# Performance work log

Measured on AMD Instinct MI355X. Metric: run time of the kernel, lower is better.

## Reference

```python
import jax, jax.numpy as jnp
import numpy as np

C = 128  # n_atom_basis


def setup_inputs() -> dict:
    key = jax.random.key(0)
    k_h, k_A, k_Ww, k_Wb, k_aw, k_ab = jax.random.split(key, 6)
    B, N = 8, 2048
    h = jax.random.normal(k_h, (B, N, C), dtype=jnp.float32)
    A = jax.random.uniform(k_A, (B, N, N), dtype=jnp.float32)
    # nn.Linear(C, C)
    lim_W = 1.0 / np.sqrt(C)
    W_w = jax.random.uniform(k_Ww, (C, C), minval=-lim_W, maxval=lim_W, dtype=jnp.float32)
    W_b = jax.random.uniform(k_Wb, (C,), minval=-lim_W, maxval=lim_W, dtype=jnp.float32)
    # nn.Linear(2C, 1)
    lim_a = 1.0 / np.sqrt(2 * C)
    a_w = jax.random.uniform(k_aw, (2 * C,), minval=-lim_a, maxval=lim_a, dtype=jnp.float32)
    a_b = jax.random.uniform(k_ab, (), minval=-lim_a, maxval=lim_a, dtype=jnp.float32)
    return {"h": h, "A": A, "W_w": W_w, "W_b": W_b, "a_w": a_w, "a_b": a_b}


def reference(h, A, W_w, W_b, a_w, a_b):
    # Wh computed once ([B,N,C]) instead of the original's redundant [B,N,N,C] broadcast.
    Wh = jnp.einsum('bnc,dc->bnd', h, W_w) + W_b
    # a([hi, hj]) = a_w[:C]@Wh_i + a_w[C:]@Wh_j + a_b  -> rank-1 decomposition of the concat-linear
    si = Wh @ a_w[:C]          # [B,N]
    sj = Wh @ a_w[C:]          # [B,N]
    s = si[:, :, None] + sj[:, None, :] + a_b  # [B,N,N] raw scores
    e = jnp.exp(s) * A                          # masked exp (no max-subtraction: matches original math)
    alpha = e / jnp.sum(e, axis=2, keepdims=True)
    # weighted sum over neighbors j of the ORIGINAL h (as in the source, not Wh)
    h_prime = jnp.einsum('bij,bjc->bic', alpha, h)
    return h_prime
```

## Files before the change

kernel.cpp:

```cpp
#include <hip/hip_runtime.h>
#include <math.h>
#include <stdint.h>

#define Bn 8
#define Nn 2048
#define Cn 128
#define CP 144
#define NKB (Nn / 32)

typedef _Float16 f16x8 __attribute__((ext_vector_type(8)));
typedef _Float16 f16x4 __attribute__((ext_vector_type(4)));
typedef _Float16 f16x2 __attribute__((ext_vector_type(2)));
typedef __fp16   fp16x2 __attribute__((ext_vector_type(2)));
typedef float    f32x4 __attribute__((ext_vector_type(4)));

__global__ __launch_bounds__(256) void prep_kernel(const float* __restrict__ Ww,
                                                   const float* __restrict__ Wb,
                                                   const float* __restrict__ aw,
                                                   float* __restrict__ vout) {
    int tid = threadIdx.x;
    if (tid < 128) {
        float acc = 0.f;
#pragma unroll 16
        for (int d = 0; d < Cn; ++d) acc += Ww[d * Cn + tid] * aw[Cn + d];
        vout[tid] = acc;
    } else if (tid < 192) {
        int i = tid - 128;
        float p = Wb[i] * aw[Cn + i] + Wb[i + 64] * aw[Cn + i + 64];
        p += __shfl_xor(p, 32, 64);
        p += __shfl_xor(p, 16, 64);
        p += __shfl_xor(p, 8, 64);
        p += __shfl_xor(p, 4, 64);
        p += __shfl_xor(p, 2, 64);
        p += __shfl_xor(p, 1, 64);
        if (i == 0) vout[128] = p;
    }
}

__global__ __launch_bounds__(256) void rows_kernel(const float* __restrict__ h,
                                                   const float* __restrict__ vout,
                                                   _Float16* __restrict__ hWt) {
    __shared__ float tile[16][132];
    __shared__ float vsh[129];
    __shared__ float wsh[16];

    int bid = blockIdx.x;
    int b   = bid & 7;
    int n0  = (bid >> 3) << 4;
    int tid = threadIdx.x;

    if (tid < 129) vsh[tid] = vout[tid];
    {
#pragma unroll
        for (int i = 0; i < 2; ++i) {
            int idx = tid + 256 * i;
            int r = idx >> 5, f4 = idx & 31;
            *(float4*)&tile[r][f4 * 4] =
                ((const float4*)(h + (size_t)(b * Nn + n0 + r) * Cn))[f4];
        }
    }
    __syncthreads();

    {
        int r = tid >> 4, g = tid & 15;
        float acc = 0.f;
#pragma unroll
        for (int ii = 0; ii < 8; ++ii) {
            int i = g * 8 + ii;
            acc += tile[r][i] * vsh[i];
        }
        acc += __shfl_xor(acc, 1, 64);
        acc += __shfl_xor(acc, 2, 64);
        acc += __shfl_xor(acc, 4, 64);
        acc += __shfl_xor(acc, 8, 64);
        if (g == 0) wsh[r] = expf(acc + vsh[128]);
    }
    __syncthreads();

    {
        int kb = n0 >> 5, khalf = (n0 >> 4) & 1;
        _Float16* hWb = hWt + ((size_t)(b * NKB + kb) * CP) * 32 + khalf * 16;
#pragma unroll
        for (int i = 0; i < 5; ++i) {
            int idx = tid + 256 * i;
            if (idx < 1152) {
                int cp = idx >> 3, p = idx & 7;
                int r0 = p * 2;
                f16x2 v2;
                if (cp < 128) {
                    v2[0] = (_Float16)(wsh[r0] * tile[r0][cp]);
                    v2[1] = (_Float16)(wsh[r0 + 1] * tile[r0 + 1][cp]);
                } else if (cp == 128) {
                    v2[0] = (_Float16)wsh[r0];
                    v2[1] = (_Float16)wsh[r0 + 1];
                } else {
                    v2[0] = (_Float16)0.f;
                    v2[1] = (_Float16)0.f;
                }
                *(f16x2*)(hWb + (size_t)cp * 32 + p * 2) = v2;
            }
        }
    }
}

__global__ __launch_bounds__(512, 4) void attn_kernel(const float* __restrict__ A,
                                                      const _Float16* __restrict__ hWt,
                                                      float* __restrict__ out) {
    __shared__ _Float16 Af[2][4][32][40];
    __shared__ float den[32];

    int bid = blockIdx.x;
    int b   = bid & 7;
    int i0  = (bid >> 3) << 5;
    int tid = threadIdx.x;
    int wv  = tid >> 6, l = tid & 63;
    int m   = l & 15, q = l >> 4;

    const float*    Ab  = A   + (size_t)(b * Nn + i0) * Nn;
    const _Float16* hWb = hWt + (size_t)b * NKB * CP * 32;

    int sr0 = tid >> 5, sf4 = tid & 31;
    const float* sgA = Ab + (size_t)sr0 * Nn + sf4 * 4;
    const float* sgB = Ab + (size_t)(sr0 + 16) * Nn + sf4 * 4;
    int sch = sf4 >> 3, skl = (sf4 & 7) * 4;

    f32x4 accc[2];
    f32x4 acc8;
    accc[0] = (f32x4){0.f, 0.f, 0.f, 0.f};
    accc[1] = (f32x4){0.f, 0.f, 0.f, 0.f};
    acc8    = (f32x4){0.f, 0.f, 0.f, 0.f};

    auto cvtst = [&](int t, int row, float4 v) {
        union { fp16x2 h2[2]; f16x4 v4; } u;
        u.h2[0] = __builtin_amdgcn_cvt_pkrtz(v.x, v.y);
        u.h2[1] = __builtin_amdgcn_cvt_pkrtz(v.z, v.w);
        *(f16x4*)&Af[t & 1][sch][row][skl] = u.v4;
    };
    auto loadB = [&](int t, f16x8* bf) {
#pragma unroll
        for (int ck = 0; ck < 4; ++ck)
            bf[ck] = *(const f16x8*)(hWb + ((size_t)(4 * t + ck) * CP + wv * 16 + m) * 32 + q * 8);
        if (wv < 2) {
#pragma unroll
            for (int ck = 0; ck < 4; ++ck)
                bf[4 + ck] = *(const f16x8*)(hWb + ((size_t)(4 * t + ck) * CP + 128 + m) * 32 + q * 8);
        }
    };
    auto compute = [&](int buf, const f16x8* bf) {
#pragma unroll
        for (int ck = 0; ck < 4; ++ck) {
            f16x8 af0 = *(const f16x8*)&Af[buf][ck][m][q * 8];
            f16x8 af1 = *(const f16x8*)&Af[buf][ck][16 + m][q * 8];
            accc[0] = __builtin_amdgcn_mfma_f32_16x16x32_f16(af0, bf[ck], accc[0], 0, 0, 0);
            accc[1] = __builtin_amdgcn_mfma_f32_16x16x32_f16(af1, bf[ck], accc[1], 0, 0, 0);
            if (wv < 2)
                acc8 = __builtin_amdgcn_mfma_f32_16x16x32_f16(wv ? af1 : af0, bf[4 + ck],
                                                              acc8, 0, 0, 0);
        }
    };

    float4 a0x = *(const float4*)(sgA);
    float4 a0y = *(const float4*)(sgB);
    float4 a1x = *(const float4*)(sgA + 128);
    float4 a1y = *(const float4*)(sgB + 128);
    f16x8 bfA[8], bfB[8];
    loadB(0, bfA);
    cvtst(0, sr0, a0x);
    cvtst(0, sr0 + 16, a0y);
    __syncthreads();

    for (int t2 = 0; t2 < 8; ++t2) {
        int te = 2 * t2, to = te + 1;
        loadB(to, bfB);
        if (t2 < 7) {
            a0x = *(const float4*)(sgA + (te + 2) * 128);
            a0y = *(const float4*)(sgB + (te + 2) * 128);
        }
        compute(0, bfA);
        cvtst(to, sr0, a1x);
        cvtst(to, sr0 + 16, a1y);
        __syncthreads();
        if (t2 < 7) {
            loadB(to + 1, bfA);
            a1x = *(const float4*)(sgA + (to + 2) * 128);
            a1y = *(const float4*)(sgB + (to + 2) * 128);
        }
        compute(1, bfB);
        if (t2 < 7) {
            cvtst(to + 1, sr0, a0x);
            cvtst(to + 1, sr0 + 16, a0y);
        }
        __syncthreads();
    }

    if (wv < 2 && m == 0) {
#pragma unroll
        for (int r = 0; r < 4; ++r) den[wv * 16 + q * 4 + r] = acc8[r];
    }
    __syncthreads();

#pragma unroll
    for (int mt = 0; mt < 2; ++mt) {
#pragma unroll
        for (int r = 0; r < 4; ++r) {
            int row = mt * 16 + q * 4 + r;
            float invd = 1.f / den[row];
            out[(size_t)(b * Nn + i0 + row) * Cn + wv * 16 + m] = accc[mt][r] * invd;
        }
    }
}

extern "C" void kernel_launch(void* const* d_in, const int* in_sizes, int n_in,
                              void* d_out, int out_size, void* d_ws, size_t ws_size,
                              hipStream_t stream) {
    const float* h  = (const float*)d_in[0];
    const float* A  = (const float*)d_in[1];
    const float* Ww = (const float*)d_in[2];
    const float* Wb = (const float*)d_in[3];
    const float* aw = (const float*)d_in[4];
    float* out = (float*)d_out;

    char* ws = (char*)d_ws;
    _Float16* hWt  = (_Float16*)ws;
    float*    vout = (float*)(ws + (size_t)Bn * NKB * CP * 32 * 2);

    prep_kernel<<<1, 256, 0, stream>>>(Ww, Wb, aw, vout);
    rows_kernel<<<Bn * (Nn / 16), 256, 0, stream>>>(h, vout, hWt);
    attn_kernel<<<Bn * (Nn / 32), 512, 0, stream>>>(A, hWt, out);
}
```

Baseline: 234.8 us.

## Feed A directly into 32x32 MFMA operands, dropping LDS staging

The attention kernel now loads each wave's A fragment straight from global memory into registers, converts it to fp16 and feeds 32x32x16 MFMAs. This removes the LDS double buffer and the per-step block barriers. Each block now covers 64 rows instead of 32, and the hW buffer's padded channel dimension grows to 160 so every 32-wide channel tile lines up. The cost is that each A row is fetched by four waves (one per channel tile), relying on cache hits, and per-lane loads are strided across rows, so coalescing is worse.

New measurement: 291.0 us. 1.24x slower.

```diff
diff --git a/kernel.cpp b/kernel.cpp
--- a/kernel.cpp
+++ b/kernel.cpp
@@ -5,14 +5,14 @@
 #define Bn 8
 #define Nn 2048
 #define Cn 128
-#define CP 144
+#define CP2 160
 #define NKB (Nn / 32)
 
 typedef _Float16 f16x8 __attribute__((ext_vector_type(8)));
 typedef _Float16 f16x4 __attribute__((ext_vector_type(4)));
 typedef _Float16 f16x2 __attribute__((ext_vector_type(2)));
 typedef __fp16   fp16x2 __attribute__((ext_vector_type(2)));
-typedef float    f32x4 __attribute__((ext_vector_type(4)));
+typedef float    f32x16 __attribute__((ext_vector_type(16)));
 
 __global__ __launch_bounds__(256) void prep_kernel(const float* __restrict__ Ww,
                                                    const float* __restrict__ Wb,
@@ -79,134 +79,84 @@
 
     {
         int kb = n0 >> 5, khalf = (n0 >> 4) & 1;
-        _Float16* hWb = hWt + ((size_t)(b * NKB + kb) * CP) * 32 + khalf * 16;
+        _Float16* hWb = hWt + ((size_t)(b * NKB + kb) * CP2) * 32 + khalf * 16;
 #pragma unroll
         for (int i = 0; i < 5; ++i) {
             int idx = tid + 256 * i;
-            if (idx < 1152) {
-                int cp = idx >> 3, p = idx & 7;
-                int r0 = p * 2;
-                f16x2 v2;
-                if (cp < 128) {
-                    v2[0] = (_Float16)(wsh[r0] * tile[r0][cp]);
-                    v2[1] = (_Float16)(wsh[r0 + 1] * tile[r0 + 1][cp]);
-                } else if (cp == 128) {
-                    v2[0] = (_Float16)wsh[r0];
-                    v2[1] = (_Float16)wsh[r0 + 1];
-                } else {
-                    v2[0] = (_Float16)0.f;
-                    v2[1] = (_Float16)0.f;
-                }
-                *(f16x2*)(hWb + (size_t)cp * 32 + p * 2) = v2;
+            int cp = idx >> 3, p = idx & 7;
+            int r0 = p * 2;
+            f16x2 v2;
+            if (cp < 128) {
+                v2[0] = (_Float16)(wsh[r0] * tile[r0][cp]);
+                v2[1] = (_Float16)(wsh[r0 + 1] * tile[r0 + 1][cp]);
+            } else if (cp == 128) {
+                v2[0] = (_Float16)wsh[r0];
+                v2[1] = (_Float16)wsh[r0 + 1];
+            } else {
+                v2[0] = (_Float16)0.f;
+                v2[1] = (_Float16)0.f;
             }
+            *(f16x2*)(hWb + (size_t)cp * 32 + p * 2) = v2;
         }
     }
 }
 
-__global__ __launch_bounds__(512, 4) void attn_kernel(const float* __restrict__ A,
+__global__ __launch_bounds__(512, 2) void attn_kernel(const float* __restrict__ A,
                                                       const _Float16* __restrict__ hWt,
                                                       float* __restrict__ out) {
-    __shared__ _Float16 Af[2][4][32][40];
-    __shared__ float den[32];
+    __shared__ float den_lds[64];
 
     int bid = blockIdx.x;
     int b   = bid & 7;
-    int i0  = (bid >> 3) << 5;
+    int i0  = (bid >> 3) << 6;
     int tid = threadIdx.x;
     int wv  = tid >> 6, l = tid & 63;
-    int m   = l & 15, q = l >> 4;
+    int mi  = wv & 1, ci = wv >> 1;
+    int n   = l & 31, kb2 = l >> 5;
 
-    const float*    Ab  = A   + (size_t)(b * Nn + i0) * Nn;
-    const _Float16* hWb = hWt + (size_t)b * NKB * CP * 32;
+    const float* Arow = A + (size_t)(b * Nn + i0 + mi * 32 + n) * Nn + kb2 * 8;
+    const _Float16* hWb = hWt + (size_t)b * NKB * CP2 * 32;
+    int cp  = ci * 32 + n;
+    int cpd = 128 + n;
 
-    int sr0 = tid >> 5, sf4 = tid & 31;
-    const float* sgA = Ab + (size_t)sr0 * Nn + sf4 * 4;
-    const float* sgB = Ab + (size_t)(sr0 + 16) * Nn + sf4 * 4;
-    int sch = sf4 >> 3, skl = (sf4 & 7) * 4;
+    f32x16 acc  = (f32x16)(0.f);
+    f32x16 dacc = (f32x16)(0.f);
+    bool do_den = (ci == 0);
 
-    f32x4 accc[2];
-    f32x4 acc8;
-    accc[0] = (f32x4){0.f, 0.f, 0.f, 0.f};
-    accc[1] = (f32x4){0.f, 0.f, 0.f, 0.f};
-    acc8    = (f32x4){0.f, 0.f, 0.f, 0.f};
+#pragma unroll 4
+    for (int kk = 0; kk < 128; ++kk) {
+        float4 x = *(const float4*)(Arow + kk * 16);
+        float4 y = *(const float4*)(Arow + kk * 16 + 4);
+        union { fp16x2 h2[4]; f16x8 v; } u;
+        u.h2[0] = __builtin_amdgcn_cvt_pkrtz(x.x, x.y);
+        u.h2[1] = __builtin_amdgcn_cvt_pkrtz(x.z, x.w);
+        u.h2[2] = __builtin_amdgcn_cvt_pkrtz(y.x, y.y);
+        u.h2[3] = __builtin_amdgcn_cvt_pkrtz(y.z, y.w);
 
-    auto cvtst = [&](int t, int row, float4 v) {
-        union { fp16x2 h2[2]; f16x4 v4; } u;
-        u.h2[0] = __builtin_amdgcn_cvt_pkrtz(v.x, v.y);
-        u.h2[1] = __builtin_amdgcn_cvt_pkrtz(v.z, v.w);
-        *(f16x4*)&Af[t & 1][sch][row][skl] = u.v4;
-    };
-    auto loadB = [&](int t, f16x8* bf) {
-#pragma unroll
-        for (int ck = 0; ck < 4; ++ck)
-            bf[ck] = *(const f16x8*)(hWb + ((size_t)(4 * t + ck) * CP + wv * 16 + m) * 32 + q * 8);
-        if (wv < 2) {
-#pragma unroll
-            for (int ck = 0; ck < 4; ++ck)
-                bf[4 + ck] = *(const f16x8*)(hWb + ((size_t)(4 * t + ck) * CP + 128 + m) * 32 + q * 8);
+        int j0 = kk * 16 + kb2 * 8;
+        const _Float16* bp = hWb + ((size_t)(j0 >> 5) * CP2) * 32 + (j0 & 31);
+        f16x8 bf = *(const f16x8*)(bp + (size_t)cp * 32);
+        acc = __builtin_amdgcn_mfma_f32_32x32x16_f16(u.v, bf, acc, 0, 0, 0);
+        if (do_den) {
+            f16x8 bd = *(const f16x8*)(bp + (size_t)cpd * 32);
+            dacc = __builtin_amdgcn_mfma_f32_32x32x16_f16(u.v, bd, dacc, 0, 0, 0);
         }
-    };
-    auto compute = [&](int buf, const f16x8* bf) {
-#pragma unroll
-        for (int ck = 0; ck < 4; ++ck) {
-            f16x8 af0 = *(const f16x8*)&Af[buf][ck][m][q * 8];
-            f16x8 af1 = *(const f16x8*)&Af[buf][ck][16 + m][q * 8];
-            accc[0] = __builtin_amdgcn_mfma_f32_16x16x32_f16(af0, bf[ck], accc[0], 0, 0, 0);
-            accc[1] = __builtin_amdgcn_mfma_f32_16x16x32_f16(af1, bf[ck], accc[1], 0, 0, 0);
-            if (wv < 2)
-                acc8 = __builtin_amdgcn_mfma_f32_16x16x32_f16(wv ? af1 : af0, bf[4 + ck],
-                                                              acc8, 0, 0, 0);
-        }
-    };
-
-    float4 a0x = *(const float4*)(sgA);
-    float4 a0y = *(const float4*)(sgB);
-    float4 a1x = *(const float4*)(sgA + 128);
-    float4 a1y = *(const float4*)(sgB + 128);
-    f16x8 bfA[8], bfB[8];
-    loadB(0, bfA);
-    cvtst(0, sr0, a0x);
-    cvtst(0, sr0 + 16, a0y);
-    __syncthreads();
-
-    for (int t2 = 0; t2 < 8; ++t2) {
-        int te = 2 * t2, to = te + 1;
-        loadB(to, bfB);
-        if (t2 < 7) {
-            a0x = *(const float4*)(sgA + (te + 2) * 128);
-            a0y = *(const float4*)(sgB + (te + 2) * 128);
-        }
-        compute(0, bfA);
-        cvtst(to, sr0, a1x);
-        cvtst(to, sr0 + 16, a1y);
-        __syncthreads();
-        if (t2 < 7) {
-            loadB(to + 1, bfA);
-            a1x = *(const float4*)(sgA + (to + 2) * 128);
-            a1y = *(const float4*)(sgB + (to + 2) * 128);
-        }
-        compute(1, bfB);
-        if (t2 < 7) {
-            cvtst(to + 1, sr0, a0x);
-            cvtst(to + 1, sr0 + 16, a0y);
-        }
-        __syncthreads();
     }
 
-    if (wv < 2 && m == 0) {
+    if (do_den && n == 0) {
 #pragma unroll
-        for (int r = 0; r < 4; ++r) den[wv * 16 + q * 4 + r] = acc8[r];
+        for (int r = 0; r < 16; ++r) {
+            int row = (r & 3) + 8 * (r >> 2) + 4 * kb2;
+            den_lds[mi * 32 + row] = dacc[r];
+        }
     }
     __syncthreads();
 
 #pragma unroll
-    for (int mt = 0; mt < 2; ++mt) {
-#pragma unroll
-        for (int r = 0; r < 4; ++r) {
-            int row = mt * 16 + q * 4 + r;
-            float invd = 1.f / den[row];
-            out[(size_t)(b * Nn + i0 + row) * Cn + wv * 16 + m] = accc[mt][r] * invd;
-        }
+    for (int r = 0; r < 16; ++r) {
+        int row = (r & 3) + 8 * (r >> 2) + 4 * kb2;
+        float inv = 1.f / den_lds[mi * 32 + row];
+        out[(size_t)(b * Nn + i0 + mi * 32 + row) * Cn + ci * 32 + n] = acc[r] * inv;
     }
 }
 
@@ -222,9 +172,9 @@
 
     char* ws = (char*)d_ws;
     _Float16* hWt  = (_Float16*)ws;
-    float*    vout = (float*)(ws + (size_t)Bn * NKB * CP * 32 * 2);
+    float*    vout = (float*)(ws + (size_t)Bn * NKB * CP2 * 32 * 2);
 
     prep_kernel<<<1, 256, 0, stream>>>(Ww, Wb, aw, vout);
     rows_kernel<<<Bn * (Nn / 16), 256, 0, stream>>>(h, vout, hWt);
-    attn_kernel<<<Bn * (Nn / 32), 512, 0, stream>>>(A, hWt, out);
+    attn_kernel<<<Bn * (Nn / 64), 512, 0, stream>>>(A, hWt, out);
 }
```
